# Optimization experiments

Measured on AMD Instinct MI355X. Metric: run time of the kernel, lower is better.

The kernel has to match this reference:

```python
import jax, jax.numpy as jnp
import numpy as np

N, PAIR, M, D, O, R = 4096, 2, 64, 128, 128, 2
MAX_DEG = 32


def setup_inputs() -> dict:
    key = jax.random.key(0)
    k1, k2, k3, k4, k5, k6 = jax.random.split(key, 6)
    node_features = jax.random.normal(k1, (N, PAIR, M, D), dtype=jnp.float32)
    deg = jax.random.randint(k2, (N,), 0, MAX_DEG, dtype=jnp.int32)
    # per-relation Linear params (stored as [in, out]) and self-loop Linear
    W_r = jax.random.normal(k3, (R, D, O), dtype=jnp.float32) / np.sqrt(D)
    b_r = jax.random.normal(k4, (R, O), dtype=jnp.float32) * 0.01
    W0 = jax.random.normal(k5, (D, O), dtype=jnp.float32) / np.sqrt(D)
    b0 = jax.random.normal(k6, (O,), dtype=jnp.float32) * 0.01
    return {"node_features": node_features, "deg": deg, "W_r": W_r,
            "b_r": b_r, "W0": W0, "b0": b0}


def reference(node_features, deg, W_r, b_r, W0, b0):
    # Original: for each relation r, for each neighbor, adds W_r(x_i);
    # i.e. sum_r deg_i * (x_i @ W_r + b_r) = deg_i * (x_i @ sum_r W_r + sum_r b_r)
    Wsum = W_r.sum(axis=0)          # [D, O]
    bsum = b_r.sum(axis=0)          # [O]
    rel = jnp.einsum('npmd,do->npmo', node_features, Wsum) + bsum
    self_term = jnp.einsum('npmd,do->npmo', node_features, W0) + b0
    d = deg.astype(node_features.dtype)[:, None, None, None]
    h = jax.nn.relu(d * rel + self_term)  # [N, 2, M, O]
    # edge representation: mm(h_i, h_j.T) per entity -> [N, M, M]
    out = jnp.einsum('nmo,nko->nmk', h[:, 0], h[:, 1])
    return out
```

## Files before the change

### kernel.cpp

```cpp
#include <hip/hip_runtime.h>
#include <hip/hip_bf16.h>


typedef __attribute__((ext_vector_type(8))) short bf16x8;
typedef __attribute__((ext_vector_type(4))) float f32x4;

__device__ __forceinline__ unsigned int pkbf(float a, float b) {
    union { __hip_bfloat162 h; unsigned int u; } v;
    v.h = __float22bfloat162_rn(float2{a, b});
    return v.u;
}

__global__ __launch_bounds__(256) void build_weights(
    const float* __restrict__ W_r,
    const float* __restrict__ b_r,
    const float* __restrict__ W0,
    const float* __restrict__ b0,
    unsigned short* __restrict__ wfrag,
    float* __restrict__ call)
{
    int t = blockIdx.x * blockDim.x + threadIdx.x;
    int lane = t & 63;
    int ks = (t >> 6) & 3;
    int ct = (t >> 8) & 7;
    int d  = (t >> 11) & 31;
    int o = ct * 16 + (lane & 15);
    int kbase = ks * 32 + (lane >> 4) * 8;
    unsigned int* dst = (unsigned int*)(wfrag + (size_t)t * 8);
#pragma unroll
    for (int j = 0; j < 4; ++j) {
        int k0 = kbase + 2 * j;
        float wA = (float)d * (W_r[k0 * 128 + o] + W_r[128 * 128 + k0 * 128 + o]) + W0[k0 * 128 + o];
        float wB = (float)d * (W_r[(k0 + 1) * 128 + o] + W_r[128 * 128 + (k0 + 1) * 128 + o]) + W0[(k0 + 1) * 128 + o];
        dst[j] = pkbf(wA, wB);
    }
    if (t < 32 * 128) {
        int dd = t >> 7, oo = t & 127;
        call[t] = (float)dd * (b_r[oo] + b_r[128 + oo]) + b0[oo];
    }
}

__global__ __launch_bounds__(256) void edge_kernel(
    const float* __restrict__ x,
    const int* __restrict__ deg,
    const unsigned short* __restrict__ wfrag,
    const float* __restrict__ call,
    float* __restrict__ out)
{
    __shared__ char ldsb[32768];

    const int n = blockIdx.x;
    const int tid = threadIdx.x;
    const int wave = tid >> 6;
    const int lane = tid & 63;
    const int l15 = lane & 15;
    const int lhi = lane >> 4;
    const int d = deg[n];

    const float* xn = x + (size_t)n * (2 * 64 * 128);
    const char* wsrc = (const char*)(wfrag + (size_t)d * (8 * 4 * 64 * 8));
    const float* cd = call + d * 128;

#pragma unroll
    for (int i = 0; i < 8; ++i) {
        __builtin_amdgcn_global_load_lds(
            (const __attribute__((address_space(1))) unsigned int*)(wsrc + (size_t)i * 4096 + (size_t)tid * 16),
            (__attribute__((address_space(3))) unsigned int*)(ldsb + i * 4096 + wave * 1024),
            16, 0, 0);
    }

    const int rbase = wave * 32;
    const float* r0p = xn + (size_t)(rbase + l15) * 128 + lhi * 8;
    const float* r1p = r0p + (size_t)16 * 128;
    bf16x8 afrag[2][4];
    f32x4 ring[4][2];
#pragma unroll
    for (int u = 0; u < 4; ++u) {
        const f32x4* p = (const f32x4*)(r0p + (u & 3) * 32);
        ring[u][0] = p[0];
        ring[u][1] = p[1];
    }
#pragma unroll
    for (int u = 0; u < 8; ++u) {
        f32x4 a0 = ring[u & 3][0];
        f32x4 a1 = ring[u & 3][1];
        if (u < 4) {
            const f32x4* p = (const f32x4*)(r1p + (u & 3) * 32);
            ring[u & 3][0] = p[0];
            ring[u & 3][1] = p[1];
        }
        union { bf16x8 vv; unsigned int uu[4]; } f;
        f.uu[0] = pkbf(a0.x, a0.y);
        f.uu[1] = pkbf(a0.z, a0.w);
        f.uu[2] = pkbf(a1.x, a1.y);
        f.uu[3] = pkbf(a1.z, a1.w);
        afrag[u >> 2][u & 3] = f.vv;
        __builtin_amdgcn_sched_barrier(0);
    }

    __syncthreads();

    f32x4 ccA = *(const f32x4*)(cd + 0 * 16 + lhi * 4);
    f32x4 ccB = *(const f32x4*)(cd + 1 * 16 + lhi * 4);
#pragma unroll
    for (int p = 0; p < 4; ++p) {
        const int ct0 = 2 * p, ct1 = 2 * p + 1;
        bf16x8 bf0[4], bf1[4];
#pragma unroll
        for (int ks = 0; ks < 4; ++ks) {
            bf0[ks] = *(const bf16x8*)(ldsb + ct0 * 4096 + ks * 1024 + lane * 16);
            bf1[ks] = *(const bf16x8*)(ldsb + ct1 * 4096 + ks * 1024 + lane * 16);
        }
        f32x4 acc0[2] = {{0.f,0.f,0.f,0.f},{0.f,0.f,0.f,0.f}};
        f32x4 acc1[2] = {{0.f,0.f,0.f,0.f},{0.f,0.f,0.f,0.f}};
#pragma unroll
        for (int ks = 0; ks < 4; ++ks) {
#pragma unroll
            for (int rt = 0; rt < 2; ++rt) {
                acc0[rt] = __builtin_amdgcn_mfma_f32_16x16x32_bf16(bf0[ks], afrag[rt][ks], acc0[rt], 0, 0, 0);
                acc1[rt] = __builtin_amdgcn_mfma_f32_16x16x32_bf16(bf1[ks], afrag[rt][ks], acc1[rt], 0, 0, 0);
            }
        }
        const int ctn = (p < 3) ? (2 * p + 2) : 0;
        f32x4 ccA_n = *(const f32x4*)(cd + ctn * 16 + lhi * 4);
        f32x4 ccB_n = *(const f32x4*)(cd + (ctn + 1) * 16 + lhi * 4);

        __syncthreads();

#pragma unroll
        for (int rt = 0; rt < 2; ++rt) {
            const int m = rbase + rt * 16 + l15;
            const int slot = ((lhi >> 1) ^ ((m >> 2) & 1));
            {
                float h0v = fmaxf(acc0[rt][0] + ccA.x, 0.f);
                float h1v = fmaxf(acc0[rt][1] + ccA.y, 0.f);
                float h2v = fmaxf(acc0[rt][2] + ccA.z, 0.f);
                float h3v = fmaxf(acc0[rt][3] + ccA.w, 0.f);
                union { unsigned int u[2]; unsigned long long ull; } pk;
                pk.u[0] = pkbf(h0v, h1v);
                pk.u[1] = pkbf(h2v, h3v);
                *(unsigned long long*)(ldsb + ct0 * 4096 + m * 32 + slot * 16 + (lhi & 1) * 8) = pk.ull;
            }
            {
                float h0v = fmaxf(acc1[rt][0] + ccB.x, 0.f);
                float h1v = fmaxf(acc1[rt][1] + ccB.y, 0.f);
                float h2v = fmaxf(acc1[rt][2] + ccB.z, 0.f);
                float h3v = fmaxf(acc1[rt][3] + ccB.w, 0.f);
                union { unsigned int u[2]; unsigned long long ull; } pk;
                pk.u[0] = pkbf(h0v, h1v);
                pk.u[1] = pkbf(h2v, h3v);
                *(unsigned long long*)(ldsb + ct1 * 4096 + m * 32 + slot * 16 + (lhi & 1) * 8) = pk.ull;
            }
        }
        ccA = ccA_n;
        ccB = ccB_n;
    }
    __syncthreads();

    const int mrow = wave * 16 + l15;
    bf16x8 hb[4];
#pragma unroll
    for (int ks = 0; ks < 4; ++ks) {
        const int ct = ks * 2 + (lhi >> 1);
        const int s  = (lhi & 1) ^ ((mrow >> 2) & 1);
        hb[ks] = *(const bf16x8*)(ldsb + ct * 4096 + mrow * 32 + s * 16);
    }
    float* outn = out + (size_t)n * 4096;
#pragma unroll
    for (int qt = 0; qt < 4; ++qt) {
        const int qrow = 64 + qt * 16 + l15;
        f32x4 acc = {0.f, 0.f, 0.f, 0.f};
#pragma unroll
        for (int ks = 0; ks < 4; ++ks) {
            const int ct = ks * 2 + (lhi >> 1);
            const int s  = (lhi & 1) ^ ((qrow >> 2) & 1);
            bf16x8 ha = *(const bf16x8*)(ldsb + ct * 4096 + qrow * 32 + s * 16);
            acc = __builtin_amdgcn_mfma_f32_16x16x32_bf16(ha, hb[ks], acc, 0, 0, 0);
        }
        *(f32x4*)(outn + mrow * 64 + qt * 16 + lhi * 4) = acc;
    }
}

extern "C" void kernel_launch(void* const* d_in, const int* in_sizes, int n_in,
                              void* d_out, int out_size, void* d_ws, size_t ws_size,
                              hipStream_t stream) {
    const float* x   = (const float*)d_in[0];
    const int*   deg = (const int*)d_in[1];
    const float* W_r = (const float*)d_in[2];
    const float* b_r = (const float*)d_in[3];
    const float* W0  = (const float*)d_in[4];
    const float* b0  = (const float*)d_in[5];
    float* out = (float*)d_out;

    unsigned short* wfrag = (unsigned short*)d_ws;
    float* call = (float*)((unsigned short*)d_ws + 32 * 8 * 4 * 64 * 8);

    build_weights<<<256, 256, 0, stream>>>(W_r, b_r, W0, b0, wfrag, call);
    edge_kernel<<<4096, 256, 0, stream>>>(x, deg, wfrag, call, out);
}
```

Baseline: 75.15 us.

## Stage bias in LDS, process one column tile per step, raise occupancy hint

The per-degree bias row is now copied into LDS with an async global-to-LDS load instead of being prefetched from global memory into registers. The main loop handles one 16-column tile per iteration instead of two, which shrinks live B-fragment and accumulator registers. A launch_bounds min-blocks hint of 4 pushes the compiler toward higher occupancy. In exchange the kernel runs twice as many __syncthreads and gets less MFMA interleaving per step, and the LDS use grows slightly.

```diff
diff --git a/kernel.cpp b/kernel.cpp
--- a/kernel.cpp
+++ b/kernel.cpp
@@ -40,14 +40,14 @@
     }
 }
 
-__global__ __launch_bounds__(256) void edge_kernel(
+__global__ __launch_bounds__(256, 4) void edge_kernel(
     const float* __restrict__ x,
     const int* __restrict__ deg,
     const unsigned short* __restrict__ wfrag,
     const float* __restrict__ call,
     float* __restrict__ out)
 {
-    __shared__ char ldsb[32768];
+    __shared__ char ldsb[33280];
 
     const int n = blockIdx.x;
     const int tid = threadIdx.x;
@@ -66,6 +66,12 @@
         __builtin_amdgcn_global_load_lds(
             (const __attribute__((address_space(1))) unsigned int*)(wsrc + (size_t)i * 4096 + (size_t)tid * 16),
             (__attribute__((address_space(3))) unsigned int*)(ldsb + i * 4096 + wave * 1024),
+            16, 0, 0);
+    }
+    if (tid < 32) {
+        __builtin_amdgcn_global_load_lds(
+            (const __attribute__((address_space(1))) unsigned int*)(cd + tid * 4),
+            (__attribute__((address_space(3))) unsigned int*)(ldsb + 32768),
             16, 0, 0);
     }
 
@@ -100,30 +106,19 @@
 
     __syncthreads();
 
-    f32x4 ccA = *(const f32x4*)(cd + 0 * 16 + lhi * 4);
-    f32x4 ccB = *(const f32x4*)(cd + 1 * 16 + lhi * 4);
 #pragma unroll
-    for (int p = 0; p < 4; ++p) {
-        const int ct0 = 2 * p, ct1 = 2 * p + 1;
-        bf16x8 bf0[4], bf1[4];
+    for (int ct = 0; ct < 8; ++ct) {
+        bf16x8 bfrag[4];
 #pragma unroll
-        for (int ks = 0; ks < 4; ++ks) {
-            bf0[ks] = *(const bf16x8*)(ldsb + ct0 * 4096 + ks * 1024 + lane * 16);
-            bf1[ks] = *(const bf16x8*)(ldsb + ct1 * 4096 + ks * 1024 + lane * 16);
-        }
-        f32x4 acc0[2] = {{0.f,0.f,0.f,0.f},{0.f,0.f,0.f,0.f}};
-        f32x4 acc1[2] = {{0.f,0.f,0.f,0.f},{0.f,0.f,0.f,0.f}};
+        for (int ks = 0; ks < 4; ++ks)
+            bfrag[ks] = *(const bf16x8*)(ldsb + ct * 4096 + ks * 1024 + lane * 16);
+        f32x4 acc[2] = {{0.f,0.f,0.f,0.f},{0.f,0.f,0.f,0.f}};
 #pragma unroll
-        for (int ks = 0; ks < 4; ++ks) {
+        for (int ks = 0; ks < 4; ++ks)
 #pragma unroll
-            for (int rt = 0; rt < 2; ++rt) {
-                acc0[rt] = __builtin_amdgcn_mfma_f32_16x16x32_bf16(bf0[ks], afrag[rt][ks], acc0[rt], 0, 0, 0);
-                acc1[rt] = __builtin_amdgcn_mfma_f32_16x16x32_bf16(bf1[ks], afrag[rt][ks], acc1[rt], 0, 0, 0);
-            }
-        }
-        const int ctn = (p < 3) ? (2 * p + 2) : 0;
-        f32x4 ccA_n = *(const f32x4*)(cd + ctn * 16 + lhi * 4);
-        f32x4 ccB_n = *(const f32x4*)(cd + (ctn + 1) * 16 + lhi * 4);
+            for (int rt = 0; rt < 2; ++rt)
+                acc[rt] = __builtin_amdgcn_mfma_f32_16x16x32_bf16(bfrag[ks], afrag[rt][ks], acc[rt], 0, 0, 0);
+        const f32x4 cc4 = *(const f32x4*)(ldsb + 32768 + ct * 64 + lhi * 16);
 
         __syncthreads();
 
@@ -131,29 +126,15 @@
         for (int rt = 0; rt < 2; ++rt) {
             const int m = rbase + rt * 16 + l15;
             const int slot = ((lhi >> 1) ^ ((m >> 2) & 1));
-            {
-                float h0v = fmaxf(acc0[rt][0] + ccA.x, 0.f);
-                float h1v = fmaxf(acc0[rt][1] + ccA.y, 0.f);
-                float h2v = fmaxf(acc0[rt][2] + ccA.z, 0.f);
-                float h3v = fmaxf(acc0[rt][3] + ccA.w, 0.f);
-                union { unsigned int u[2]; unsigned long long ull; } pk;
-                pk.u[0] = pkbf(h0v, h1v);
-                pk.u[1] = pkbf(h2v, h3v);
-                *(unsigned long long*)(ldsb + ct0 * 4096 + m * 32 + slot * 16 + (lhi & 1) * 8) = pk.ull;
-            }
-            {
-                float h0v = fmaxf(acc1[rt][0] + ccB.x, 0.f);
-                float h1v = fmaxf(acc1[rt][1] + ccB.y, 0.f);
-                float h2v = fmaxf(acc1[rt][2] + ccB.z, 0.f);
-                float h3v = fmaxf(acc1[rt][3] + ccB.w, 0.f);
-                union { unsigned int u[2]; unsigned long long ull; } pk;
-                pk.u[0] = pkbf(h0v, h1v);
-                pk.u[1] = pkbf(h2v, h3v);
-                *(unsigned long long*)(ldsb + ct1 * 4096 + m * 32 + slot * 16 + (lhi & 1) * 8) = pk.ull;
-            }
+            float h0v = fmaxf(acc[rt][0] + cc4.x, 0.f);
+            float h1v = fmaxf(acc[rt][1] + cc4.y, 0.f);
+            float h2v = fmaxf(acc[rt][2] + cc4.z, 0.f);
+            float h3v = fmaxf(acc[rt][3] + cc4.w, 0.f);
+            union { unsigned int u[2]; unsigned long long ull; } pk;
+            pk.u[0] = pkbf(h0v, h1v);
+            pk.u[1] = pkbf(h2v, h3v);
+            *(unsigned long long*)(ldsb + ct * 4096 + m * 32 + slot * 16 + (lhi & 1) * 8) = pk.ull;
         }
-        ccA = ccA_n;
-        ccB = ccB_n;
     }
     __syncthreads();
 
```

Measured after the change: 74.99 us. Within noise of the previous version (-0.2%).
